# Performance work log

Hardware: AMD Instinct MI355X
Metric: run time of the kernel (lower is better)

The kernel has to match this reference:

```python
import jax, jax.numpy as jnp
import numpy as np

H = 1024   # hidden_size
A = 16     # num_actions
T = 64     # time steps
N = 128    # batch (parallel envs)


def setup_inputs() -> dict:
    key = jax.random.key(0)
    ks = jax.random.split(key, 16)
    s = 0.02  # small-ish init scale for weights
    a_idx = jax.random.randint(ks[5], (T, N), 0, A)
    return {
        "x": jax.random.normal(ks[0], (T * N, H), jnp.float32),
        "hxs_gru": jax.random.normal(ks[1], (N, H), jnp.float32),
        "hxs_p": jax.random.normal(ks[2], (N, 2 * H), jnp.float32),
        # masks are 0/1 episode-reset flags
        "masks": jax.random.bernoulli(ks[3], 0.95, (T * N, 1)).astype(jnp.float32),
        "prev_action_one_hot": jax.nn.one_hot(a_idx, A, dtype=jnp.float32),
        "w_ih": jax.random.normal(ks[6], (3 * H, H), jnp.float32) * s,
        "w_hh": jax.random.normal(ks[7], (3 * H, H), jnp.float32) * s,
        "b_ih": jnp.zeros((3 * H,), jnp.float32),
        "b_hh": jnp.zeros((3 * H,), jnp.float32),
        "p_w1": jax.random.normal(ks[8], (2 * H, 2 * H + A), jnp.float32) * s,
        "p_b1": jnp.zeros((2 * H,), jnp.float32),
        "p_w2": jax.random.normal(ks[9], (H, 2 * H), jnp.float32) * s,
        "p_b2": jnp.zeros((H,), jnp.float32),
        "mu_w": jax.random.normal(ks[10], (H, H), jnp.float32) * s,
        "mu_b": jnp.zeros((H,), jnp.float32),
        "lv_w": jax.random.normal(ks[11], (H, H), jnp.float32) * s,
        "lv_b": jnp.zeros((H,), jnp.float32),
    }


def reference(x, hxs_gru, hxs_p, masks, prev_action_one_hot,
              w_ih, w_hh, b_ih, b_hh,
              p_w1, p_b1, p_w2, p_b2,
              mu_w, mu_b, lv_w, lv_b):
    n = hxs_gru.shape[0]
    h_dim = hxs_gru.shape[1]
    t = x.shape[0] // n
    xT = x.reshape(t, n, h_dim)        # [T,N,H]
    mT = masks.reshape(t, n, 1)        # [T,N,1]

    # ---- _forward_gru: masked GRUCell recurrence over time ----
    def gru_step(h, inp):
        x_t, m_t = inp
        h0 = h * m_t                                  # per-step state reset
        gi = x_t @ w_ih.T + b_ih                      # [N,3H]
        gh = h0 @ w_hh.T + b_hh                       # [N,3H]
        ir, iz, inn = jnp.split(gi, 3, axis=1)
        hr, hz, hn = jnp.split(gh, 3, axis=1)
        r = jax.nn.sigmoid(ir + hr)
        z = jax.nn.sigmoid(iz + hz)
        nn_ = jnp.tanh(inn + r * hn)
        h_new = (1.0 - z) * nn_ + z * h0              # PyTorch GRUCell update
        return h_new, h_new

    gru_hxs, gru_acc = jax.lax.scan(gru_step, hxs_gru, (xT, mT))
    gru_acc = gru_acc.reshape(t * n, h_dim)

    # ---- _forward_p_gru: MLP recurrence with mask-gated state/action ----
    def p_step(h, inp):
        x_t, m_t, a_t = inp
        hidden = h * m_t + jnp.concatenate([x_t, x_t], axis=1) * (1.0 - m_t)
        cur = jnp.concatenate([a_t * m_t, hidden], axis=1)   # [N, A+2H]
        d = jax.nn.relu(cur @ p_w1.T + p_b1)                 # [N, 2H]
        d = jax.nn.relu(d @ p_w2.T + p_b2)                   # [N, H]
        mu = d @ mu_w.T + mu_b                               # [N, H]
        lv = d @ lv_w.T + lv_b                               # [N, H]
        h_new = jnp.concatenate([mu, x_t], axis=1)           # [N, 2H]
        return h_new, (mu, lv)

    # note: original concatenates action first: cat((a*m, hidden))
    p_hxs, (p_mu, p_lv) = jax.lax.scan(p_step, hxs_p, (xT, mT, prev_action_one_hot))
    p_mu = p_mu.reshape(t * n, h_dim)
    p_lv = p_lv.reshape(t * n, h_dim)
    return (gru_acc, gru_hxs, p_mu, p_lv, p_hxs)
```

## Files before the change

kernel.cpp:

```cpp
#include <hip/hip_runtime.h>

typedef unsigned int uint;
typedef unsigned short ushort;
typedef __bf16 bf16x8_t __attribute__((ext_vector_type(8)));
typedef float f32x4_t __attribute__((ext_vector_type(4)));
typedef uint u32x4_t __attribute__((ext_vector_type(4)));

__device__ __forceinline__ ushort f2b(float f) {
    uint u = __builtin_bit_cast(uint, f);
    u += 0x7fffu + ((u >> 16) & 1u);
    return (ushort)(u >> 16);
}
__device__ __forceinline__ float b2f(ushort h) {
    return __builtin_bit_cast(float, (uint)h << 16);
}
__device__ __forceinline__ float sigm(float v) { return 1.f / (1.f + __expf(-v)); }
__device__ __forceinline__ float tanh_(float v) {
    v = fmaxf(-15.f, fminf(15.f, v));
    float e = __expf(2.f * v);
    return (e - 1.f) / (e + 1.f);
}

__device__ __forceinline__ uint ld_cg_u32(const uint* p) {
    uint r;
    asm volatile("global_load_dword %0, %1, off sc0 sc1\n\ts_waitcnt vmcnt(0)"
                 : "=v"(r) : "v"(p) : "memory");
    return r;
}
__device__ __forceinline__ void st_cg_u32(uint* p, uint v) {
    asm volatile("global_store_dword %0, %1, off sc0 sc1" :: "v"(p), "v"(v) : "memory");
}
__device__ __forceinline__ void st_cg_u16(ushort* p, uint v) {
    asm volatile("global_store_short %0, %1, off sc0 sc1" :: "v"(p), "v"(v) : "memory");
}
__device__ __forceinline__ void st_cg_x4(ushort* p, u32x4_t v) {
    asm volatile("global_store_dwordx4 %0, %1, off sc0 sc1" :: "v"(p), "v"(v) : "memory");
}
__device__ __forceinline__ void ld8_nc(uint4 u[8],
    const void* p0, const void* p1, const void* p2, const void* p3,
    const void* p4, const void* p5, const void* p6, const void* p7)
{
    asm volatile(
        "global_load_dwordx4 %0, %8, off\n\t"
        "global_load_dwordx4 %1, %9, off\n\t"
        "global_load_dwordx4 %2, %10, off\n\t"
        "global_load_dwordx4 %3, %11, off\n\t"
        "global_load_dwordx4 %4, %12, off\n\t"
        "global_load_dwordx4 %5, %13, off\n\t"
        "global_load_dwordx4 %6, %14, off\n\t"
        "global_load_dwordx4 %7, %15, off"
        : "=&v"(u[0]), "=&v"(u[1]), "=&v"(u[2]), "=&v"(u[3]),
          "=&v"(u[4]), "=&v"(u[5]), "=&v"(u[6]), "=&v"(u[7])
        : "v"(p0), "v"(p1), "v"(p2), "v"(p3), "v"(p4), "v"(p5), "v"(p6), "v"(p7)
        : "memory");
}
__device__ __forceinline__ void vm0() {
    asm volatile("s_waitcnt vmcnt(0)" ::: "memory");
    __builtin_amdgcn_sched_barrier(0);
}
__device__ __forceinline__ bf16x8_t u2b(uint4 u) { return __builtin_bit_cast(bf16x8_t, u); }

#define SMEM_BYTES 36864
union U8 { ushort h[8]; uint4 v; };

template<int BN, int EPI, bool AF32>
__device__ __forceinline__ void gemm_body(
    int bx, int by, const void* Av, int lda,
    const ushort* Bp, int ldb, int K,
    void* Ov, int ldo, const float* bias, char* smem)
{
    constexpr int LDW = 72;
    ushort* As = (ushort*)smem;
    ushort* Bs = (ushort*)(smem + 128 * LDW * 2);
    const int tid = threadIdx.x, lane = tid & 63, wid = tid >> 6;
    constexpr int WC = (BN == 128) ? 2 : 1;
    constexpr int WR = 4 / WC;
    constexpr int WROWS = 128 / WR;
    constexpr int WCOLS = BN / WC;
    constexpr int MI = WROWS / 16, NI = WCOLS / 16;
    const int wr = (WC == 2) ? (wid >> 1) : wid;
    const int wc = (WC == 2) ? (wid & 1) : 0;
    const int row0 = by * 128, col0 = bx * BN;

    f32x4_t acc[MI][NI];
#pragma unroll
    for (int i = 0; i < MI; i++)
#pragma unroll
        for (int j = 0; j < NI; j++) acc[i][j] = (f32x4_t){0.f, 0.f, 0.f, 0.f};

    for (int k0 = 0; k0 < K; k0 += 64) {
        __syncthreads();
#pragma unroll
        for (int cc = 0; cc < 4; cc++) {
            int chunk = tid + cc * 256;
            int r = chunk >> 3, c8 = chunk & 7;
            uint4 val;
            if constexpr (AF32) {
                const float* Af = (const float*)Av + (size_t)(row0 + r) * lda + k0 + c8 * 8;
                float4 v0 = ((const float4*)Af)[0];
                float4 v1 = ((const float4*)Af)[1];
                U8 u;
                u.h[0] = f2b(v0.x); u.h[1] = f2b(v0.y); u.h[2] = f2b(v0.z); u.h[3] = f2b(v0.w);
                u.h[4] = f2b(v1.x); u.h[5] = f2b(v1.y); u.h[6] = f2b(v1.z); u.h[7] = f2b(v1.w);
                val = u.v;
            } else {
                val = *(const uint4*)((const ushort*)Av + (size_t)(row0 + r) * lda + k0 + c8 * 8);
            }
            *(uint4*)&As[r * LDW + c8 * 8] = val;
        }
#pragma unroll
        for (int cc = 0; cc < BN / 32; cc++) {
            int chunk = tid + cc * 256;
            int r = chunk >> 3, c8 = chunk & 7;
            uint4 val = *(const uint4*)(Bp + (size_t)(col0 + r) * ldb + k0 + c8 * 8);
            *(uint4*)&Bs[r * LDW + c8 * 8] = val;
        }
        __syncthreads();
#pragma unroll
        for (int kk = 0; kk < 64; kk += 32) {
            int ko = kk + ((lane >> 4) << 3);
            bf16x8_t af[MI], bf[NI];
#pragma unroll
            for (int mi = 0; mi < MI; mi++)
                af[mi] = *(const bf16x8_t*)&As[(wr * WROWS + mi * 16 + (lane & 15)) * LDW + ko];
#pragma unroll
            for (int ni = 0; ni < NI; ni++)
                bf[ni] = *(const bf16x8_t*)&Bs[(wc * WCOLS + ni * 16 + (lane & 15)) * LDW + ko];
#pragma unroll
            for (int mi = 0; mi < MI; mi++)
#pragma unroll
                for (int ni = 0; ni < NI; ni++)
                    acc[mi][ni] = __builtin_amdgcn_mfma_f32_16x16x32_bf16(af[mi], bf[ni], acc[mi][ni], 0, 0, 0);
        }
    }
#pragma unroll
    for (int mi = 0; mi < MI; mi++) {
#pragma unroll
        for (int ni = 0; ni < NI; ni++) {
            int gcol = col0 + wc * WCOLS + ni * 16 + (lane & 15);
#pragma unroll
            for (int i = 0; i < 4; i++) {
                int grow = row0 + wr * WROWS + mi * 16 + ((lane >> 4) << 2) + i;
                float v = acc[mi][ni][i];
                if constexpr (EPI == 0) {
                    ((float*)Ov)[(size_t)grow * ldo + gcol] = v + bias[gcol];
                } else if constexpr (EPI == 1) {
                    ((ushort*)Ov)[(size_t)grow * ldo + gcol] = f2b(v);
                } else if constexpr (EPI == 2) {
                    ((ushort*)Ov)[(size_t)grow * ldo + gcol] = f2b(v + bias[gcol]);
                } else if constexpr (EPI == 3) {
                    int t = grow >> 7, row = grow & 127;
                    int g = gcol >> 10, cb = (gcol & 1023) >> 4, c16 = gcol & 15;
                    ((ushort*)Ov)[(((size_t)t * 3 + g) * 64 + cb) * 2048 + row * 16 + c16] = f2b(v);
                } else {
                    int t = grow >> 7, row = grow & 127;
                    int cg = gcol >> 5, c32 = gcol & 31;
                    ((ushort*)Ov)[((size_t)t * 64 + cg) * 4096 + row * 32 + c32] = f2b(v + bias[gcol]);
                }
            }
        }
    }
}

template<int BN, int EPI, bool AF32>
__global__ __launch_bounds__(256) void gemm_k(
    const void* A, int lda, const ushort* B, int ldb, int K,
    void* O, int ldo, const float* bias)
{
    __shared__ char smem[SMEM_BYTES];
    gemm_body<BN, EPI, AF32>(blockIdx.x, blockIdx.y, A, lda, B, ldb, K, O, ldo, bias, smem);
}

#define NFLAG_G 0
#define NFLAG_A 4096
#define NFLAG_B 12288
#define NFLAGS  20480

__device__ __forceinline__ void wg_wait(uint* f, int n, int tid) {
    if (tid < n) {
        while (ld_cg_u32(f + tid) == 0u) __builtin_amdgcn_s_sleep(1);
    }
    __syncthreads();
}
__device__ __forceinline__ void wg_arrive(uint* slot, int tid) {
    __syncthreads();
    if (tid == 0) st_cg_u32(slot, 1u);
}

__device__ void role_gru(int cb, const ushort* __restrict__ whhb, ushort* hb,
                         const ushort* __restrict__ gi, const float* masks,
                         const float* b_ih, const float* b_hh, const float* hxs_g,
                         float* out, uint* flags, char* lds)
{
    const int tid = threadIdx.x, lane = tid & 63, w = tid >> 6;
    const int colL = cb * 16 + (lane & 15);
    const int kw = w * 256;
    const int kl = (lane >> 4) << 3;

    bf16x8_t bw[3][8];
#pragma unroll
    for (int g = 0; g < 3; g++)
#pragma unroll
        for (int ks = 0; ks < 8; ks++)
            bw[g][ks] = *(const bf16x8_t*)(whhb + (size_t)(g * 1024 + colL) * 1024 + kw + ks * 32 + kl);

    const float bihr = b_ih[colL], bihz = b_ih[1024 + colL], bihn = b_ih[2048 + colL];
    const float bhhr = b_hh[colL], bhhz = b_hh[1024 + colL], bhhn = b_hh[2048 + colL];

    f32x4_t hown[2];
#pragma unroll
    for (int j = 0; j < 2; j++)
#pragma unroll
        for (int i = 0; i < 4; i++)
            hown[j][i] = hxs_g[(size_t)((2 * w + j) * 16 + ((lane >> 4) << 2) + i) * 1024 + colL];

    for (int t = 0; t < 64; t++) {
        float mc[2][4], mn[2][4], g0p[2][4], g1p[2][4], g2p[2][4];
        const size_t gb = ((size_t)t * 3 * 64 + cb) * 2048;
#pragma unroll
        for (int j = 0; j < 2; j++) {
            const int rt = 2 * w + j;
#pragma unroll
            for (int i = 0; i < 4; i++) {
                const int row = rt * 16 + ((lane >> 4) << 2) + i;
                mc[j][i] = masks[t * 128 + row];
                mn[j][i] = (t < 63) ? masks[(t + 1) * 128 + row] : 0.f;
                g0p[j][i] = b2f(gi[gb + row * 16 + (lane & 15)]);
                g1p[j][i] = b2f(gi[gb + 131072 + row * 16 + (lane & 15)]);
                g2p[j][i] = b2f(gi[gb + 262144 + row * 16 + (lane & 15)]);
            }
        }
        if (t) wg_wait(flags + NFLAG_G + (t - 1) * 64, 64, tid);
        const ushort* base = hb + (size_t)t * 131072 + (size_t)(lane & 15) * 1024 + kw + kl;
        f32x4_t acc[3][8];
#pragma unroll
        for (int g = 0; g < 3; g++)
#pragma unroll
            for (int rt = 0; rt < 8; rt++) acc[g][rt] = (f32x4_t){0.f, 0.f, 0.f, 0.f};
#pragma unroll
        for (int half = 0; half < 2; half++) {
            const ushort* b = base + half * 128;
            uint4 u0[8], u1[8], u2[8], u3[8];
            ld8_nc(u0, b, b + 16384, b + 32768, b + 49152, b + 65536, b + 81920, b + 98304, b + 114688);
            ld8_nc(u1, b + 32, b + 16384 + 32, b + 32768 + 32, b + 49152 + 32, b + 65536 + 32, b + 81920 + 32, b + 98304 + 32, b + 114688 + 32);
            ld8_nc(u2, b + 64, b + 16384 + 64, b + 32768 + 64, b + 49152 + 64, b + 65536 + 64, b + 81920 + 64, b + 98304 + 64, b + 114688 + 64);
            ld8_nc(u3, b + 96, b + 16384 + 96, b + 32768 + 96, b + 49152 + 96, b + 65536 + 96, b + 81920 + 96, b + 98304 + 96, b + 114688 + 96);
            vm0();
#pragma unroll
            for (int g = 0; g < 3; g++)
#pragma unroll
                for (int rt = 0; rt < 8; rt++) {
                    acc[g][rt] = __builtin_amdgcn_mfma_f32_16x16x32_bf16(u2b(u0[rt]), bw[g][half * 4 + 0], acc[g][rt], 0, 0, 0);
                    acc[g][rt] = __builtin_amdgcn_mfma_f32_16x16x32_bf16(u2b(u1[rt]), bw[g][half * 4 + 1], acc[g][rt], 0, 0, 0);
                    acc[g][rt] = __builtin_amdgcn_mfma_f32_16x16x32_bf16(u2b(u2[rt]), bw[g][half * 4 + 2], acc[g][rt], 0, 0, 0);
                    acc[g][rt] = __builtin_amdgcn_mfma_f32_16x16x32_bf16(u2b(u3[rt]), bw[g][half * 4 + 3], acc[g][rt], 0, 0, 0);
                }
        }
#pragma unroll
        for (int g = 0; g < 3; g++)
#pragma unroll
            for (int rt = 0; rt < 8; rt++)
                *(f32x4_t*)(lds + ((size_t)(w * 24 + g * 8 + rt) * 64 + lane) * 16) = acc[g][rt];
        __syncthreads();
#pragma unroll
        for (int j = 0; j < 2; j++) {
            const int rt = 2 * w + j;
            f32x4_t sg[3];
#pragma unroll
            for (int g = 0; g < 3; g++) {
                sg[g] = (f32x4_t){0.f, 0.f, 0.f, 0.f};
#pragma unroll
                for (int ww = 0; ww < 4; ww++)
                    sg[g] += *(const f32x4_t*)(lds + ((size_t)(ww * 24 + g * 8 + rt) * 64 + lane) * 16);
            }
#pragma unroll
            for (int i = 0; i < 4; i++) {
                const int row = rt * 16 + ((lane >> 4) << 2) + i;
                const float h0 = hown[j][i] * mc[j][i];
                const float rv = sigm(g0p[j][i] + bihr + bhhr + sg[0][i]);
                const float zv = sigm(g1p[j][i] + bihz + bhhz + sg[1][i]);
                const float nv = tanh_(g2p[j][i] + bihn + rv * (sg[2][i] + bhhn));
                const float hnew = (1.f - zv) * nv + zv * h0;
                out[(size_t)(t * 128 + row) * 1024 + colL] = hnew;
                hown[j][i] = hnew;
                if (t < 63)
                    st_cg_u16(hb + (size_t)(t + 1) * 131072 + (size_t)row * 1024 + colL,
                              (uint)f2b(hnew * mn[j][i]));
            }
        }
        wg_arrive(flags + NFLAG_G + t * 64 + cb, tid);
    }
}

__device__ void role_p(int p, const ushort* __restrict__ Wcb, const ushort* __restrict__ w1h1b,
                       const ushort* __restrict__ hp1b, const ushort* __restrict__ w2b,
                       const ushort* __restrict__ d1pre, const float* masks, const float* cvec,
                       const float* p_b2, ushort* d1r, ushort* d2r, uint* flags, char* lds)
{
    const int tid = threadIdx.x, lane = tid & 63, w = tid >> 6;
    const int rowg = p >> 6, colg = p & 63;
    const int rA0 = rowg * 64, cA0 = colg * 32;
    const int rB0 = rowg * 64, cB0 = colg * 16;
    const int kwA = w * 256, kwB = w * 512, kl = (lane >> 4) << 3;
    ushort* stg = (ushort*)(lds + 32768) + w * 512;

    bf16x8_t wcF[2][8];
#pragma unroll
    for (int ct = 0; ct < 2; ct++)
#pragma unroll
        for (int ks = 0; ks < 8; ks++)
            wcF[ct][ks] = *(const bf16x8_t*)(Wcb + (size_t)(cA0 + ct * 16 + (lane & 15)) * 1024 + kwA + ks * 32 + kl);
    bf16x8_t w2F[16];
#pragma unroll
    for (int ks = 0; ks < 16; ks++)
        w2F[ks] = *(const bf16x8_t*)(w2b + (size_t)(cB0 + (lane & 15)) * 2048 + kwB + ks * 32 + kl);
    const float cv0 = cvec[cA0 + (lane & 15)], cv1 = cvec[cA0 + 16 + (lane & 15)];
    const float pb = p_b2[cB0 + (lane & 15)];

    for (int t = 0; t < 64; t++) {
        float mA[4], preA[2][4];
        const size_t pbase = ((size_t)t * 64 + colg) * 4096;
#pragma unroll
        for (int i = 0; i < 4; i++) {
            const int row = rA0 + w * 16 + ((lane >> 4) << 2) + i;
            mA[i] = masks[t * 128 + row];
            preA[0][i] = b2f(d1pre[pbase + (row & 127) * 32 + (lane & 15)]);
            preA[1][i] = b2f(d1pre[pbase + (row & 127) * 32 + 16 + (lane & 15)]);
        }
        if (t) wg_wait(flags + NFLAG_B + (t - 1) * 128 + rowg * 64, 64, tid);
        f32x4_t accA[2][4];
#pragma unroll
        for (int ct = 0; ct < 2; ct++)
#pragma unroll
            for (int rt = 0; rt < 4; rt++) accA[ct][rt] = (f32x4_t){0.f, 0.f, 0.f, 0.f};
        if (t == 0) {
#pragma unroll
            for (int ks = 0; ks < 8; ks++) {
                bf16x8_t af[4], b0[2];
#pragma unroll
                for (int ct = 0; ct < 2; ct++)
                    b0[ct] = *(const bf16x8_t*)(w1h1b + (size_t)(cA0 + ct * 16 + (lane & 15)) * 1024 + kwA + ks * 32 + kl);
#pragma unroll
                for (int rt = 0; rt < 4; rt++)
                    af[rt] = *(const bf16x8_t*)(hp1b + (size_t)(rA0 + rt * 16 + (lane & 15)) * 1024 + kwA + ks * 32 + kl);
#pragma unroll
                for (int ct = 0; ct < 2; ct++)
#pragma unroll
                    for (int rt = 0; rt < 4; rt++)
                        accA[ct][rt] = __builtin_amdgcn_mfma_f32_16x16x32_bf16(af[rt], b0[ct], accA[ct][rt], 0, 0, 0);
            }
        } else {
            const ushort* Ab = d2r + (size_t)(t - 1) * 131072 + (size_t)(rA0 + (lane & 15)) * 1024 + kwA + kl;
            uint4 u0[8], u1[8], u2[8], u3[8];
            ld8_nc(u0, Ab,       Ab + 16384,       Ab + 32768,       Ab + 49152,       Ab + 32,  Ab + 16384 + 32,  Ab + 32768 + 32,  Ab + 49152 + 32);
            ld8_nc(u1, Ab + 64,  Ab + 16384 + 64,  Ab + 32768 + 64,  Ab + 49152 + 64,  Ab + 96,  Ab + 16384 + 96,  Ab + 32768 + 96,  Ab + 49152 + 96);
            ld8_nc(u2, Ab + 128, Ab + 16384 + 128, Ab + 32768 + 128, Ab + 49152 + 128, Ab + 160, Ab + 16384 + 160, Ab + 32768 + 160, Ab + 49152 + 160);
            ld8_nc(u3, Ab + 192, Ab + 16384 + 192, Ab + 32768 + 192, Ab + 49152 + 192, Ab + 224, Ab + 16384 + 224, Ab + 32768 + 224, Ab + 49152 + 224);
            vm0();
#pragma unroll
            for (int ct = 0; ct < 2; ct++)
#pragma unroll
                for (int rt = 0; rt < 4; rt++) {
                    accA[ct][rt] = __builtin_amdgcn_mfma_f32_16x16x32_bf16(u2b(u0[rt]), wcF[ct][0], accA[ct][rt], 0, 0, 0);
                    accA[ct][rt] = __builtin_amdgcn_mfma_f32_16x16x32_bf16(u2b(u0[4 + rt]), wcF[ct][1], accA[ct][rt], 0, 0, 0);
                    accA[ct][rt] = __builtin_amdgcn_mfma_f32_16x16x32_bf16(u2b(u1[rt]), wcF[ct][2], accA[ct][rt], 0, 0, 0);
                    accA[ct][rt] = __builtin_amdgcn_mfma_f32_16x16x32_bf16(u2b(u1[4 + rt]), wcF[ct][3], accA[ct][rt], 0, 0, 0);
                    accA[ct][rt] = __builtin_amdgcn_mfma_f32_16x16x32_bf16(u2b(u2[rt]), wcF[ct][4], accA[ct][rt], 0, 0, 0);
                    accA[ct][rt] = __builtin_amdgcn_mfma_f32_16x16x32_bf16(u2b(u2[4 + rt]), wcF[ct][5], accA[ct][rt], 0, 0, 0);
                    accA[ct][rt] = __builtin_amdgcn_mfma_f32_16x16x32_bf16(u2b(u3[rt]), wcF[ct][6], accA[ct][rt], 0, 0, 0);
                    accA[ct][rt] = __builtin_amdgcn_mfma_f32_16x16x32_bf16(u2b(u3[4 + rt]), wcF[ct][7], accA[ct][rt], 0, 0, 0);
                }
        }
        __syncthreads();
#pragma unroll
        for (int ct = 0; ct < 2; ct++)
#pragma unroll
            for (int rt = 0; rt < 4; rt++)
                *(f32x4_t*)(lds + ((size_t)(w * 8 + ct * 4 + rt) * 64 + lane) * 16) = accA[ct][rt];
        __syncthreads();
#pragma unroll
        for (int ct = 0; ct < 2; ct++) {
            f32x4_t s = (f32x4_t){0.f, 0.f, 0.f, 0.f};
#pragma unroll
            for (int ww = 0; ww < 4; ww++)
                s += *(const f32x4_t*)(lds + ((size_t)(ww * 8 + ct * 4 + w) * 64 + lane) * 16);
            const float cvt = (t == 0) ? 0.f : (ct ? cv1 : cv0);
#pragma unroll
            for (int i = 0; i < 4; i++) {
                float f = preA[ct][i] + mA[i] * (s[i] + cvt);
                stg[(((lane >> 4) << 2) + i) * 32 + ct * 16 + (lane & 15)] = f2b(f > 0.f ? f : 0.f);
            }
        }
        __syncthreads();
        {
            const int rl = lane >> 2, c8 = (lane & 3) * 8;
            u32x4_t v = *(const u32x4_t*)&stg[rl * 32 + c8];
            st_cg_x4(d1r + (size_t)t * 262144 + (size_t)(rA0 + w * 16 + rl) * 2048 + cA0 + c8, v);
        }
        wg_arrive(flags + NFLAG_A + t * 128 + p, tid);
        wg_wait(flags + NFLAG_A + t * 128 + rowg * 64, 64, tid);
        f32x4_t accB[4];
#pragma unroll
        for (int rt = 0; rt < 4; rt++) accB[rt] = (f32x4_t){0.f, 0.f, 0.f, 0.f};
        const ushort* Bb = d1r + (size_t)t * 262144 + (size_t)(rB0 + (lane & 15)) * 2048 + kwB + kl;
#pragma unroll
        for (int half = 0; half < 2; half++) {
            const ushort* b = Bb + half * 256;
            uint4 u0[8], u1[8], u2[8], u3[8];
            ld8_nc(u0, b,       b + 32768,       b + 65536,       b + 98304,       b + 32,  b + 32768 + 32,  b + 65536 + 32,  b + 98304 + 32);
            ld8_nc(u1, b + 64,  b + 32768 + 64,  b + 65536 + 64,  b + 98304 + 64,  b + 96,  b + 32768 + 96,  b + 65536 + 96,  b + 98304 + 96);
            ld8_nc(u2, b + 128, b + 32768 + 128, b + 65536 + 128, b + 98304 + 128, b + 160, b + 32768 + 160, b + 65536 + 160, b + 98304 + 160);
            ld8_nc(u3, b + 192, b + 32768 + 192, b + 65536 + 192, b + 98304 + 192, b + 224, b + 32768 + 224, b + 65536 + 224, b + 98304 + 224);
            vm0();
#pragma unroll
            for (int rt = 0; rt < 4; rt++) {
                accB[rt] = __builtin_amdgcn_mfma_f32_16x16x32_bf16(u2b(u0[rt]), w2F[half * 8 + 0], accB[rt], 0, 0, 0);
                accB[rt] = __builtin_amdgcn_mfma_f32_16x16x32_bf16(u2b(u0[4 + rt]), w2F[half * 8 + 1], accB[rt], 0, 0, 0);
                accB[rt] = __builtin_amdgcn_mfma_f32_16x16x32_bf16(u2b(u1[rt]), w2F[half * 8 + 2], accB[rt], 0, 0, 0);
                accB[rt] = __builtin_amdgcn_mfma_f32_16x16x32_bf16(u2b(u1[4 + rt]), w2F[half * 8 + 3], accB[rt], 0, 0, 0);
                accB[rt] = __builtin_amdgcn_mfma_f32_16x16x32_bf16(u2b(u2[rt]), w2F[half * 8 + 4], accB[rt], 0, 0, 0);
                accB[rt] = __builtin_amdgcn_mfma_f32_16x16x32_bf16(u2b(u2[4 + rt]), w2F[half * 8 + 5], accB[rt], 0, 0, 0);
                accB[rt] = __builtin_amdgcn_mfma_f32_16x16x32_bf16(u2b(u3[rt]), w2F[half * 8 + 6], accB[rt], 0, 0, 0);
                accB[rt] = __builtin_amdgcn_mfma_f32_16x16x32_bf16(u2b(u3[4 + rt]), w2F[half * 8 + 7], accB[rt], 0, 0, 0);
            }
        }
        __syncthreads();
#pragma unroll
        for (int rt = 0; rt < 4; rt++)
            *(f32x4_t*)(lds + ((size_t)(w * 4 + rt) * 64 + lane) * 16) = accB[rt];
        __syncthreads();
        {
            f32x4_t s = (f32x4_t){0.f, 0.f, 0.f, 0.f};
#pragma unroll
            for (int ww = 0; ww < 4; ww++)
                s += *(const f32x4_t*)(lds + ((size_t)(ww * 4 + w) * 64 + lane) * 16);
#pragma unroll
            for (int i = 0; i < 4; i++) {
                float f = s[i] + pb;
                stg[(((lane >> 4) << 2) + i) * 16 + (lane & 15)] = f2b(f > 0.f ? f : 0.f);
            }
        }
        __syncthreads();
        {
            if (lane < 32) {
                const int rl = lane >> 1, c8 = (lane & 1) * 8;
                u32x4_t v = *(const u32x4_t*)&stg[rl * 16 + c8];
                st_cg_x4(d2r + (size_t)t * 131072 + (size_t)(rB0 + w * 16 + rl) * 1024 + cB0 + c8, v);
            }
        }
        wg_arrive(flags + NFLAG_B + t * 128 + p, tid);
    }
}

__global__ __launch_bounds__(256, 1) void persist_k(
    const ushort* whhb, const ushort* Wcb, const ushort* w1h1b, const ushort* w2b,
    const ushort* gi, const ushort* d1pre, const ushort* hp1b,
    ushort* hb, ushort* d1r, ushort* d2r,
    const float* masks, const float* b_ih, const float* b_hh,
    const float* cvec, const float* p_b2, const float* hxs_g,
    float* out, uint* flags)
{
    __shared__ __align__(16) char lds[98304];
    const int wg = blockIdx.x;
    if (wg < 64) role_gru(wg, whhb, hb, gi, masks, b_ih, b_hh, hxs_g, out, flags, lds);
    else         role_p(wg - 64, Wcb, w1h1b, hp1b, w2b, d1pre, masks, cvec, p_b2, d1r, d2r, flags, lds);
}

__global__ void prep_w(const float* w_ih, const float* w_hh, const float* p_w1,
                       const float* p_w2, const float* mu_w, const float* lv_w,
                       ushort* wihb, ushort* whhb, ushort* w2b, ushort* muwb,
                       ushort* lvwb, ushort* muwTb, ushort* w1h1b, ushort* pw1b)
{
    const long total = 17956864;
    for (long idx = (long)blockIdx.x * 256 + threadIdx.x; idx < total; idx += (long)gridDim.x * 256) {
        long l = idx;
        if (l < 3145728) { wihb[l] = f2b(w_ih[l]); continue; } l -= 3145728;
        if (l < 3145728) { whhb[l] = f2b(w_hh[l]); continue; } l -= 3145728;
        if (l < 2097152) { w2b[l] = f2b(p_w2[l]); continue; } l -= 2097152;
        if (l < 1048576) { muwb[l] = f2b(mu_w[l]); continue; } l -= 1048576;
        if (l < 1048576) { lvwb[l] = f2b(lv_w[l]); continue; } l -= 1048576;
        if (l < 1048576) {
            int c = (int)(l >> 10), o = (int)(l & 1023);
            muwTb[l] = f2b(mu_w[(size_t)o * 1024 + c]); continue;
        } l -= 1048576;
        if (l < 2097152) {
            int r = (int)(l >> 10), c = (int)(l & 1023);
            w1h1b[l] = f2b(p_w1[(size_t)r * 2064 + 16 + c]); continue;
        } l -= 2097152;
        {
            int r = (int)(l / 2112), c = (int)(l - (long)r * 2112);
            pw1b[l] = (c < 2064) ? f2b(p_w1[(size_t)r * 2064 + c]) : (ushort)0;
        }
    }
}

__global__ void prep_x(const float* x, const float* hxs_g, const float* hxs_p,
                       const float* masks, const float* oh,
                       ushort* ain, ushort* hb0, ushort* hp1b)
{
    const long totA = 8192L * 2112, totH = 131072, totP = 131072;
    for (long idx = (long)blockIdx.x * 256 + threadIdx.x; idx < totA + totH + totP; idx += (long)gridDim.x * 256) {
        if (idx < totA) {
            long j = idx;
            int i = (int)(j / 2112);
            int c = (int)(j - (long)i * 2112);
            float m = masks[i];
            float v;
            if (c < 16) v = oh[(size_t)i * 16 + c] * m;
            else if (c < 1040) v = x[(size_t)i * 1024 + (c - 16)] * (1.f - m);
            else if (c < 2064) {
                int cc = c - 1040;
                float xp = (i >= 128) ? x[(size_t)(i - 128) * 1024 + cc]
                                      : hxs_p[(size_t)i * 2048 + 1024 + cc];
                v = xp * m + x[(size_t)i * 1024 + cc] * (1.f - m);
            } else v = 0.f;
            ain[j] = f2b(v);
            continue;
        }
        long j = idx - totA;
        if (j < totH) {
            int row = (int)(j >> 10), c = (int)(j & 1023);
            hb0[j] = f2b(hxs_g[(size_t)row * 1024 + c] * masks[row]);
            continue;
        }
        j -= totH;
        {
            int row = (int)(j >> 10), c = (int)(j & 1023);
            hp1b[j] = f2b(hxs_p[(size_t)row * 2048 + c]);
        }
    }
}

__global__ void k_cvec(const float* p_w1, const float* mu_b, float* cvec)
{
    int j = blockIdx.x * 4 + (threadIdx.x >> 6);
    int lane = threadIdx.x & 63;
    float s = 0.f;
    for (int o = lane; o < 1024; o += 64) s += p_w1[(size_t)j * 2064 + 16 + o] * mu_b[o];
#pragma unroll
    for (int off = 32; off; off >>= 1) s += __shfl_down(s, off);
    if (lane == 0) cvec[j] = s;
}

__global__ void init_flags(uint* flags)
{
    int i = blockIdx.x * 256 + threadIdx.x;
    if (i < NFLAGS) flags[i] = 0u;
}

__global__ void k_tail(float* out, const float* x)
{
    const long total = 131072 + 262144;
    for (long idx = (long)blockIdx.x * 256 + threadIdx.x; idx < total; idx += (long)gridDim.x * 256) {
        if (idx < 131072) {
            out[8388608 + idx] = out[8257536 + idx];
        } else {
            long j = idx - 131072;
            int n = (int)(j >> 11), c = (int)(j & 2047);
            out[25296896 + j] = (c < 1024)
                ? out[8519680 + (size_t)(8064 + n) * 1024 + c]
                : x[(size_t)(8064 + n) * 1024 + (c - 1024)];
        }
    }
}

extern "C" void kernel_launch(void* const* d_in, const int* in_sizes, int n_in,
                              void* d_out, int out_size, void* d_ws, size_t ws_size,
                              hipStream_t stream)
{
    (void)in_sizes; (void)n_in; (void)out_size; (void)ws_size;
    const float* x      = (const float*)d_in[0];
    const float* hxs_g  = (const float*)d_in[1];
    const float* hxs_p  = (const float*)d_in[2];
    const float* masks  = (const float*)d_in[3];
    const float* oh     = (const float*)d_in[4];
    const float* w_ih   = (const float*)d_in[5];
    const float* w_hh   = (const float*)d_in[6];
    const float* b_ih   = (const float*)d_in[7];
    const float* b_hh   = (const float*)d_in[8];
    const float* p_w1   = (const float*)d_in[9];
    const float* p_b1   = (const float*)d_in[10];
    const float* p_w2   = (const float*)d_in[11];
    const float* p_b2   = (const float*)d_in[12];
    const float* mu_w   = (const float*)d_in[13];
    const float* mu_b   = (const float*)d_in[14];
    const float* lv_w   = (const float*)d_in[15];
    const float* lv_b   = (const float*)d_in[16];
    float* out = (float*)d_out;

    char* w = (char*)d_ws;
    ushort* gi     = (ushort*)(w + 0);
    ushort* ain    = (ushort*)(w + 0);
    ushort* d1pre  = (ushort*)(w + 50331648);
    ushort* wihb   = (ushort*)(w + 83886080);
    ushort* whhb   = (ushort*)(w + 90177536);
    ushort* pw1b   = (ushort*)(w + 96468992);
    ushort* w1h1b  = (ushort*)(w + 105119744);
    ushort* w2b    = (ushort*)(w + 109314048);
    ushort* muwb   = (ushort*)(w + 113508352);
    ushort* muwTb  = (ushort*)(w + 115605504);
    ushort* lvwb   = (ushort*)(w + 117702656);
    ushort* Wcb    = (ushort*)(w + 119799808);
    ushort* hp1b   = (ushort*)(w + 123994112);
    ushort* hb     = (ushort*)(w + 124256256);
    ushort* d1r    = (ushort*)(w + 141033472);
    ushort* d2r    = (ushort*)(w + 174587904);
    float*  cvec   = (float*) (w + 191365120);
    uint*   flags  = (uint*)  (w + 191373312);

    prep_w<<<dim3(2048), 256, 0, stream>>>(w_ih, w_hh, p_w1, p_w2, mu_w, lv_w,
                                           wihb, whhb, w2b, muwb, lvwb, muwTb, w1h1b, pw1b);
    prep_x<<<dim3(4096), 256, 0, stream>>>(x, hxs_g, hxs_p, masks, oh, ain, hb, hp1b);
    k_cvec<<<dim3(512), 256, 0, stream>>>(p_w1, mu_b, cvec);
    init_flags<<<dim3(80), 256, 0, stream>>>(flags);

    gemm_k<128, 4, false><<<dim3(16, 64), 256, 0, stream>>>(
        ain, 2112, pw1b, 2112, 2112, d1pre, 0, p_b1);
    gemm_k<128, 3, true><<<dim3(24, 64), 256, 0, stream>>>(
        x, 1024, wihb, 1024, 1024, gi, 0, nullptr);
    gemm_k<128, 1, false><<<dim3(8, 16), 256, 0, stream>>>(
        w1h1b, 1024, muwTb, 1024, 1024, Wcb, 1024, nullptr);

    persist_k<<<dim3(192), 256, 0, stream>>>(
        whhb, Wcb, w1h1b, w2b, gi, d1pre, hp1b, hb, d1r, d2r,
        masks, b_ih, b_hh, cvec, p_b2, hxs_g, out, flags);

    gemm_k<128, 0, false><<<dim3(8, 64), 256, 0, stream>>>(
        d2r, 1024, muwb, 1024, 1024, out + 8519680, 1024, mu_b);
    gemm_k<128, 0, false><<<dim3(8, 64), 256, 0, stream>>>(
        d2r, 1024, lvwb, 1024, 1024, out + 16908288, 1024, lv_b);

    k_tail<<<dim3(1536), 256, 0, stream>>>(out, x);
}
```

Baseline: 1.410 ms.

## Merge prep and GEMM launches and switch to per-wave flag waits

Four prep kernels (weight conversion, input conversion, cvec, flag init) become one grid-stride kernel, and the gi GEMM, Wcb GEMM and cvec reduction share a single launch that dispatches on block index. In the persistent recurrent kernel, each wave now spins only on the 16 flags it depends on, with no sleep, instead of a workgroup-wide wait plus barrier. A __syncthreads is added before the LDS reduction to keep it correct. The aim is fewer launches and a shorter serial synchronisation path per timestep, at the cost of busier spinning on the flag memory.

Result: slower. 1.452 ms (+3.0%).

```diff
diff --git a/kernel.cpp b/kernel.cpp
--- a/kernel.cpp
+++ b/kernel.cpp
@@ -171,16 +171,39 @@
     gemm_body<BN, EPI, AF32>(blockIdx.x, blockIdx.y, A, lda, B, ldb, K, O, ldo, bias, smem);
 }
 
+__global__ __launch_bounds__(256) void gemm_rest_k(
+    const void* A1, const ushort* B1, void* O1,
+    const void* A2, const ushort* B2, void* O2,
+    const float* p_w1, const float* mu_b, float* cvec)
+{
+    __shared__ char smem[SMEM_BYTES];
+    int b = blockIdx.x;
+    if (b < 1536) {
+        gemm_body<128, 3, true>(b % 24, b / 24, A1, 1024, B1, 1024, 1024, O1, 0, nullptr, smem);
+    } else if (b < 1664) {
+        int c = b - 1536;
+        gemm_body<128, 1, false>(c & 7, c >> 3, A2, 1024, B2, 1024, 1024, O2, 1024, nullptr, smem);
+    } else {
+        int j = (b - 1664) * 4 + (threadIdx.x >> 6);
+        int lane = threadIdx.x & 63;
+        float s = 0.f;
+        for (int o = lane; o < 1024; o += 64) s += p_w1[(size_t)j * 2064 + 16 + o] * mu_b[o];
+#pragma unroll
+        for (int off = 32; off; off >>= 1) s += __shfl_down(s, off);
+        if (lane == 0) cvec[j] = s;
+    }
+}
+
 #define NFLAG_G 0
 #define NFLAG_A 4096
 #define NFLAG_B 12288
 #define NFLAGS  20480
 
-__device__ __forceinline__ void wg_wait(uint* f, int n, int tid) {
-    if (tid < n) {
-        while (ld_cg_u32(f + tid) == 0u) __builtin_amdgcn_s_sleep(1);
-    }
-    __syncthreads();
+__device__ __forceinline__ void wv_wait16(uint* f, int lane) {
+    if (lane < 16) {
+        while (ld_cg_u32(f + lane) == 0u) {}
+    }
+    __builtin_amdgcn_sched_barrier(0);
 }
 __device__ __forceinline__ void wg_arrive(uint* slot, int tid) {
     __syncthreads();
@@ -230,7 +253,7 @@
                 g2p[j][i] = b2f(gi[gb + 262144 + row * 16 + (lane & 15)]);
             }
         }
-        if (t) wg_wait(flags + NFLAG_G + (t - 1) * 64, 64, tid);
+        if (t) wv_wait16(flags + NFLAG_G + (t - 1) * 64 + w * 16, lane);
         const ushort* base = hb + (size_t)t * 131072 + (size_t)(lane & 15) * 1024 + kw + kl;
         f32x4_t acc[3][8];
 #pragma unroll
@@ -256,6 +279,7 @@
                     acc[g][rt] = __builtin_amdgcn_mfma_f32_16x16x32_bf16(u2b(u3[rt]), bw[g][half * 4 + 3], acc[g][rt], 0, 0, 0);
                 }
         }
+        __syncthreads();
 #pragma unroll
         for (int g = 0; g < 3; g++)
 #pragma unroll
@@ -327,7 +351,7 @@
             preA[0][i] = b2f(d1pre[pbase + (row & 127) * 32 + (lane & 15)]);
             preA[1][i] = b2f(d1pre[pbase + (row & 127) * 32 + 16 + (lane & 15)]);
         }
-        if (t) wg_wait(flags + NFLAG_B + (t - 1) * 128 + rowg * 64, 64, tid);
+        if (t) wv_wait16(flags + NFLAG_B + (t - 1) * 128 + rowg * 64 + w * 16, lane);
         f32x4_t accA[2][4];
 #pragma unroll
         for (int ct = 0; ct < 2; ct++)
@@ -398,7 +422,7 @@
             st_cg_x4(d1r + (size_t)t * 262144 + (size_t)(rA0 + w * 16 + rl) * 2048 + cA0 + c8, v);
         }
         wg_arrive(flags + NFLAG_A + t * 128 + p, tid);
-        wg_wait(flags + NFLAG_A + t * 128 + rowg * 64, 64, tid);
+        wv_wait16(flags + NFLAG_A + t * 128 + rowg * 64 + w * 16, lane);
         f32x4_t accB[4];
 #pragma unroll
         for (int rt = 0; rt < 4; rt++) accB[rt] = (f32x4_t){0.f, 0.f, 0.f, 0.f};
@@ -466,12 +490,17 @@
     else         role_p(wg - 64, Wcb, w1h1b, hp1b, w2b, d1pre, masks, cvec, p_b2, d1r, d2r, flags, lds);
 }
 
-__global__ void prep_w(const float* w_ih, const float* w_hh, const float* p_w1,
-                       const float* p_w2, const float* mu_w, const float* lv_w,
-                       ushort* wihb, ushort* whhb, ushort* w2b, ushort* muwb,
-                       ushort* lvwb, ushort* muwTb, ushort* w1h1b, ushort* pw1b)
-{
-    const long total = 17956864;
+__global__ void prep_all(const float* w_ih, const float* w_hh, const float* p_w1,
+                         const float* p_w2, const float* mu_w, const float* lv_w,
+                         const float* x, const float* hxs_g, const float* hxs_p,
+                         const float* masks, const float* oh,
+                         ushort* wihb, ushort* whhb, ushort* w2b, ushort* muwb,
+                         ushort* lvwb, ushort* muwTb, ushort* w1h1b, ushort* pw1b,
+                         ushort* ain, ushort* hb0, ushort* hp1b, uint* flags)
+{
+    const long totW = 17956864;
+    const long totA = 8192L * 2112, totH = 131072, totP = 131072;
+    const long total = totW + totA + totH + totP + NFLAGS;
     for (long idx = (long)blockIdx.x * 256 + threadIdx.x; idx < total; idx += (long)gridDim.x * 256) {
         long l = idx;
         if (l < 3145728) { wihb[l] = f2b(w_ih[l]); continue; } l -= 3145728;
@@ -487,23 +516,14 @@
             int r = (int)(l >> 10), c = (int)(l & 1023);
             w1h1b[l] = f2b(p_w1[(size_t)r * 2064 + 16 + c]); continue;
         } l -= 2097152;
-        {
+        if (l < 4325376) {
             int r = (int)(l / 2112), c = (int)(l - (long)r * 2112);
             pw1b[l] = (c < 2064) ? f2b(p_w1[(size_t)r * 2064 + c]) : (ushort)0;
-        }
-    }
-}
-
-__global__ void prep_x(const float* x, const float* hxs_g, const float* hxs_p,
-                       const float* masks, const float* oh,
-                       ushort* ain, ushort* hb0, ushort* hp1b)
-{
-    const long totA = 8192L * 2112, totH = 131072, totP = 131072;
-    for (long idx = (long)blockIdx.x * 256 + threadIdx.x; idx < totA + totH + totP; idx += (long)gridDim.x * 256) {
-        if (idx < totA) {
-            long j = idx;
-            int i = (int)(j / 2112);
-            int c = (int)(j - (long)i * 2112);
+            continue;
+        } l -= 4325376;
+        if (l < totA) {
+            int i = (int)(l / 2112);
+            int c = (int)(l - (long)i * 2112);
             float m = masks[i];
             float v;
             if (c < 16) v = oh[(size_t)i * 16 + c] * m;
@@ -514,38 +534,21 @@
                                       : hxs_p[(size_t)i * 2048 + 1024 + cc];
                 v = xp * m + x[(size_t)i * 1024 + cc] * (1.f - m);
             } else v = 0.f;
-            ain[j] = f2b(v);
+            ain[l] = f2b(v);
             continue;
-        }
-        long j = idx - totA;
-        if (j < totH) {
-            int row = (int)(j >> 10), c = (int)(j & 1023);
-            hb0[j] = f2b(hxs_g[(size_t)row * 1024 + c] * masks[row]);
+        } l -= totA;
+        if (l < totH) {
+            int row = (int)(l >> 10), c = (int)(l & 1023);
+            hb0[l] = f2b(hxs_g[(size_t)row * 1024 + c] * masks[row]);
             continue;
-        }
-        j -= totH;
-        {
-            int row = (int)(j >> 10), c = (int)(j & 1023);
-            hp1b[j] = f2b(hxs_p[(size_t)row * 2048 + c]);
-        }
-    }
-}
-
-__global__ void k_cvec(const float* p_w1, const float* mu_b, float* cvec)
-{
-    int j = blockIdx.x * 4 + (threadIdx.x >> 6);
-    int lane = threadIdx.x & 63;
-    float s = 0.f;
-    for (int o = lane; o < 1024; o += 64) s += p_w1[(size_t)j * 2064 + 16 + o] * mu_b[o];
-#pragma unroll
-    for (int off = 32; off; off >>= 1) s += __shfl_down(s, off);
-    if (lane == 0) cvec[j] = s;
-}
-
-__global__ void init_flags(uint* flags)
-{
-    int i = blockIdx.x * 256 + threadIdx.x;
-    if (i < NFLAGS) flags[i] = 0u;
+        } l -= totH;
+        if (l < totP) {
+            int row = (int)(l >> 10), c = (int)(l & 1023);
+            hp1b[l] = f2b(hxs_p[(size_t)row * 2048 + c]);
+            continue;
+        } l -= totP;
+        flags[l] = 0u;
+    }
 }
 
 __global__ void k_tail(float* out, const float* x)
@@ -608,18 +611,14 @@
     float*  cvec   = (float*) (w + 191365120);
     uint*   flags  = (uint*)  (w + 191373312);
 
-    prep_w<<<dim3(2048), 256, 0, stream>>>(w_ih, w_hh, p_w1, p_w2, mu_w, lv_w,
-                                           wihb, whhb, w2b, muwb, lvwb, muwTb, w1h1b, pw1b);
-    prep_x<<<dim3(4096), 256, 0, stream>>>(x, hxs_g, hxs_p, masks, oh, ain, hb, hp1b);
-    k_cvec<<<dim3(512), 256, 0, stream>>>(p_w1, mu_b, cvec);
-    init_flags<<<dim3(80), 256, 0, stream>>>(flags);
+    prep_all<<<dim3(6144), 256, 0, stream>>>(
+        w_ih, w_hh, p_w1, p_w2, mu_w, lv_w, x, hxs_g, hxs_p, masks, oh,
+        wihb, whhb, w2b, muwb, lvwb, muwTb, w1h1b, pw1b, ain, hb, hp1b, flags);
 
     gemm_k<128, 4, false><<<dim3(16, 64), 256, 0, stream>>>(
         ain, 2112, pw1b, 2112, 2112, d1pre, 0, p_b1);
-    gemm_k<128, 3, true><<<dim3(24, 64), 256, 0, stream>>>(
-        x, 1024, wihb, 1024, 1024, gi, 0, nullptr);
-    gemm_k<128, 1, false><<<dim3(8, 16), 256, 0, stream>>>(
-        w1h1b, 1024, muwTb, 1024, 1024, Wcb, 1024, nullptr);
+    gemm_rest_k<<<dim3(2176), 256, 0, stream>>>(
+        x, wihb, gi, w1h1b, muwTb, Wcb, p_w1, mu_b, cvec);
 
     persist_k<<<dim3(192), 256, 0, stream>>>(
         whhb, Wcb, w1h1b, w2b, gi, d1pre, hp1b, hb, d1r, d2r,
```
